# Performance work log

Hardware: AMD Instinct MI355X
Metric: run time of the kernel (lower is better)

Reference implementation:

```python
import jax, jax.numpy as jnp
import numpy as np

CLAMP_MIN = 1e-12
CLAMP_MAX = 1e12


def setup_inputs() -> dict:
    key = jax.random.key(0)
    k1, k2, k3 = jax.random.split(key, 3)
    N, D, C = 16384, 512, 10000
    features = jax.random.normal(k1, (N, D), dtype=jnp.float32)
    labels = jax.random.randint(k2, (N, 2), 0, C, dtype=jnp.int64)
    # torch.rand -> uniform [0,1)
    centers = jax.random.uniform(k3, (C, D), dtype=jnp.float32)
    return {"features": features, "labels": labels, "centers": centers}


def reference(features, labels, centers):
    # labels[:, -1] selects the class id per sample
    cls = labels[:, -1]
    # Original computes full cdist(features, centers)**2 then masks to the
    # label-matched entry per row. Mathematically that is ||f_i - c_{y_i}||^2,
    # so we gather the matching center and reduce directly (O(N*D)).
    c = centers[cls]                      # [N, D] gather
    diff = features - c                   # [N, D]
    d2 = jnp.sum(diff * diff, axis=-1)    # [N] squared L2 distance
    d2 = jnp.clip(d2, CLAMP_MIN, CLAMP_MAX)
    return jnp.mean(d2)
```

## Files before the change

### kernel.cpp

```cpp
#include <hip/hip_runtime.h>

#define N_ROWS 16384
#define DIM 512
#define NBLK 2048
#define NTHR 256
#define WAVES_PER_BLK (NTHR / 64)
#define ROWS_PER_WAVE 2


__global__ __launch_bounds__(NTHR, 8) void centerloss_partial(
    const float* __restrict__ features,
    const int* __restrict__ labels,
    const float* __restrict__ centers,
    float* __restrict__ partials)
{
    const int lane = threadIdx.x & 63;
    const int wid  = threadIdx.x >> 6;
    const int gwave = blockIdx.x * WAVES_PER_BLK + wid;
    const int base  = gwave * ROWS_PER_WAVE;

    int cls0 = labels[(base + 0) * 2 + 1];
    int cls1 = labels[(base + 1) * 2 + 1];

    const float4* __restrict__ f4 =
        reinterpret_cast<const float4*>(features + (size_t)base * DIM);
    float4 fa0 = f4[lane +   0];  float4 fb0 = f4[lane +  64];
    float4 fa1 = f4[lane + 128];  float4 fb1 = f4[lane + 192];

    const float4* __restrict__ c0 =
        reinterpret_cast<const float4*>(centers + (size_t)cls0 * DIM);
    const float4* __restrict__ c1 =
        reinterpret_cast<const float4*>(centers + (size_t)cls1 * DIM);
    float4 ca0 = c0[lane];  float4 cb0 = c0[lane + 64];
    float4 ca1 = c1[lane];  float4 cb1 = c1[lane + 64];

    float lsum = 0.f, dx;
    dx = fa0.x - ca0.x; lsum += dx * dx;
    dx = fa0.y - ca0.y; lsum += dx * dx;
    dx = fa0.z - ca0.z; lsum += dx * dx;
    dx = fa0.w - ca0.w; lsum += dx * dx;
    dx = fb0.x - cb0.x; lsum += dx * dx;
    dx = fb0.y - cb0.y; lsum += dx * dx;
    dx = fb0.z - cb0.z; lsum += dx * dx;
    dx = fb0.w - cb0.w; lsum += dx * dx;

    dx = fa1.x - ca1.x; lsum += dx * dx;
    dx = fa1.y - ca1.y; lsum += dx * dx;
    dx = fa1.z - ca1.z; lsum += dx * dx;
    dx = fa1.w - ca1.w; lsum += dx * dx;
    dx = fb1.x - cb1.x; lsum += dx * dx;
    dx = fb1.y - cb1.y; lsum += dx * dx;
    dx = fb1.z - cb1.z; lsum += dx * dx;
    dx = fb1.w - cb1.w; lsum += dx * dx;

    #pragma unroll
    for (int off = 1; off < 64; off <<= 1)
        lsum += __shfl_xor(lsum, off, 64);

    __shared__ float smem[WAVES_PER_BLK];
    if (lane == 0) smem[wid] = lsum;
    __syncthreads();
    if (threadIdx.x == 0) {
        float b = 0.f;
        #pragma unroll
        for (int w = 0; w < WAVES_PER_BLK; ++w) b += smem[w];
        partials[blockIdx.x] = b;
    }
}

__global__ __launch_bounds__(256) void centerloss_final(
    const float* __restrict__ partials, float* __restrict__ out)
{
    float s = 0.f;
    #pragma unroll
    for (int k = 0; k < NBLK / 256; ++k)
        s += partials[threadIdx.x + k * 256];

    #pragma unroll
    for (int off = 1; off < 64; off <<= 1)
        s += __shfl_xor(s, off, 64);

    __shared__ float smem[4];
    const int lane = threadIdx.x & 63;
    const int wave = threadIdx.x >> 6;
    if (lane == 0) smem[wave] = s;
    __syncthreads();
    if (threadIdx.x == 0) {
        float t = smem[0] + smem[1] + smem[2] + smem[3];
        out[0] = t / (float)N_ROWS;
    }
}

extern "C" void kernel_launch(void* const* d_in, const int* in_sizes, int n_in,
                              void* d_out, int out_size, void* d_ws, size_t ws_size,
                              hipStream_t stream)
{
    const float* features = (const float*)d_in[0];
    const int*   labels   = (const int*)d_in[1];
    const float* centers  = (const float*)d_in[2];
    float* out = (float*)d_out;
    float* partials = (float*)d_ws;

    centerloss_partial<<<NBLK, NTHR, 0, stream>>>(features, labels, centers, partials);
    centerloss_final<<<1, 256, 0, stream>>>(partials, out);
}
```

Baseline: 16.92 us.

## Use single-wave blocks with four rows each and nontemporal feature loads

The partial kernel now runs one 64-thread wave per block and has each wave process four rows instead of two, which removes the LDS reduction and the block barrier. Feature loads use nontemporal hints so the streamed data does not pollute the cache, and the squared differences accumulate in a 4-wide vector before a final horizontal add. The final kernel reads the 4096 partials as float4. In exchange, more loads are in flight per wave but there are fewer waves in total, and single-wave blocks may limit occupancy per CU.

```diff
diff --git a/kernel.cpp b/kernel.cpp
--- a/kernel.cpp
+++ b/kernel.cpp
@@ -2,79 +2,80 @@
 
 #define N_ROWS 16384
 #define DIM 512
-#define NBLK 2048
-#define NTHR 256
-#define WAVES_PER_BLK (NTHR / 64)
-#define ROWS_PER_WAVE 2
+#define NBLK 4096
+#define ROWS_PER_WAVE 4
+
+typedef float f32x4 __attribute__((ext_vector_type(4)));
 
 
-__global__ __launch_bounds__(NTHR, 8) void centerloss_partial(
+__global__ __launch_bounds__(64) void centerloss_partial(
     const float* __restrict__ features,
     const int* __restrict__ labels,
     const float* __restrict__ centers,
     float* __restrict__ partials)
 {
-    const int lane = threadIdx.x & 63;
-    const int wid  = threadIdx.x >> 6;
-    const int gwave = blockIdx.x * WAVES_PER_BLK + wid;
-    const int base  = gwave * ROWS_PER_WAVE;
+    const int lane = threadIdx.x;
+    const int base = blockIdx.x * ROWS_PER_WAVE;
 
     int cls0 = labels[(base + 0) * 2 + 1];
     int cls1 = labels[(base + 1) * 2 + 1];
+    int cls2 = labels[(base + 2) * 2 + 1];
+    int cls3 = labels[(base + 3) * 2 + 1];
 
-    const float4* __restrict__ f4 =
-        reinterpret_cast<const float4*>(features + (size_t)base * DIM);
-    float4 fa0 = f4[lane +   0];  float4 fb0 = f4[lane +  64];
-    float4 fa1 = f4[lane + 128];  float4 fb1 = f4[lane + 192];
+    const f32x4* __restrict__ f4 =
+        reinterpret_cast<const f32x4*>(features + (size_t)base * DIM);
+    f32x4 fa0 = __builtin_nontemporal_load(&f4[lane +   0]);
+    f32x4 fb0 = __builtin_nontemporal_load(&f4[lane +  64]);
+    f32x4 fa1 = __builtin_nontemporal_load(&f4[lane + 128]);
+    f32x4 fb1 = __builtin_nontemporal_load(&f4[lane + 192]);
+    f32x4 fa2 = __builtin_nontemporal_load(&f4[lane + 256]);
+    f32x4 fb2 = __builtin_nontemporal_load(&f4[lane + 320]);
+    f32x4 fa3 = __builtin_nontemporal_load(&f4[lane + 384]);
+    f32x4 fb3 = __builtin_nontemporal_load(&f4[lane + 448]);
 
-    const float4* __restrict__ c0 =
-        reinterpret_cast<const float4*>(centers + (size_t)cls0 * DIM);
-    const float4* __restrict__ c1 =
-        reinterpret_cast<const float4*>(centers + (size_t)cls1 * DIM);
-    float4 ca0 = c0[lane];  float4 cb0 = c0[lane + 64];
-    float4 ca1 = c1[lane];  float4 cb1 = c1[lane + 64];
+    const f32x4* __restrict__ c0 =
+        reinterpret_cast<const f32x4*>(centers + (size_t)cls0 * DIM);
+    const f32x4* __restrict__ c1 =
+        reinterpret_cast<const f32x4*>(centers + (size_t)cls1 * DIM);
+    const f32x4* __restrict__ c2 =
+        reinterpret_cast<const f32x4*>(centers + (size_t)cls2 * DIM);
+    const f32x4* __restrict__ c3 =
+        reinterpret_cast<const f32x4*>(centers + (size_t)cls3 * DIM);
+    f32x4 ca0 = c0[lane];  f32x4 cb0 = c0[lane + 64];
+    f32x4 ca1 = c1[lane];  f32x4 cb1 = c1[lane + 64];
+    f32x4 ca2 = c2[lane];  f32x4 cb2 = c2[lane + 64];
+    f32x4 ca3 = c3[lane];  f32x4 cb3 = c3[lane + 64];
 
-    float lsum = 0.f, dx;
-    dx = fa0.x - ca0.x; lsum += dx * dx;
-    dx = fa0.y - ca0.y; lsum += dx * dx;
-    dx = fa0.z - ca0.z; lsum += dx * dx;
-    dx = fa0.w - ca0.w; lsum += dx * dx;
-    dx = fb0.x - cb0.x; lsum += dx * dx;
-    dx = fb0.y - cb0.y; lsum += dx * dx;
-    dx = fb0.z - cb0.z; lsum += dx * dx;
-    dx = fb0.w - cb0.w; lsum += dx * dx;
+    f32x4 d;
+    f32x4 vsum;
+    d = fa0 - ca0; vsum  = d * d;
+    d = fb0 - cb0; vsum += d * d;
+    d = fa1 - ca1; vsum += d * d;
+    d = fb1 - cb1; vsum += d * d;
+    d = fa2 - ca2; vsum += d * d;
+    d = fb2 - cb2; vsum += d * d;
+    d = fa3 - ca3; vsum += d * d;
+    d = fb3 - cb3; vsum += d * d;
 
-    dx = fa1.x - ca1.x; lsum += dx * dx;
-    dx = fa1.y - ca1.y; lsum += dx * dx;
-    dx = fa1.z - ca1.z; lsum += dx * dx;
-    dx = fa1.w - ca1.w; lsum += dx * dx;
-    dx = fb1.x - cb1.x; lsum += dx * dx;
-    dx = fb1.y - cb1.y; lsum += dx * dx;
-    dx = fb1.z - cb1.z; lsum += dx * dx;
-    dx = fb1.w - cb1.w; lsum += dx * dx;
+    float lsum = vsum.x + vsum.y + vsum.z + vsum.w;
 
     #pragma unroll
     for (int off = 1; off < 64; off <<= 1)
         lsum += __shfl_xor(lsum, off, 64);
 
-    __shared__ float smem[WAVES_PER_BLK];
-    if (lane == 0) smem[wid] = lsum;
-    __syncthreads();
-    if (threadIdx.x == 0) {
-        float b = 0.f;
-        #pragma unroll
-        for (int w = 0; w < WAVES_PER_BLK; ++w) b += smem[w];
-        partials[blockIdx.x] = b;
-    }
+    if (lane == 0) partials[blockIdx.x] = lsum;
 }
 
 __global__ __launch_bounds__(256) void centerloss_final(
     const float* __restrict__ partials, float* __restrict__ out)
 {
+    const float4* __restrict__ p4 = reinterpret_cast<const float4*>(partials);
     float s = 0.f;
     #pragma unroll
-    for (int k = 0; k < NBLK / 256; ++k)
-        s += partials[threadIdx.x + k * 256];
+    for (int k = 0; k < NBLK / 4 / 256; ++k) {
+        float4 v = p4[threadIdx.x + k * 256];
+        s += v.x + v.y + v.z + v.w;
+    }
 
     #pragma unroll
     for (int off = 1; off < 64; off <<= 1)
@@ -101,6 +102,6 @@
     float* out = (float*)d_out;
     float* partials = (float*)d_ws;
 
-    centerloss_partial<<<NBLK, NTHR, 0, stream>>>(features, labels, centers, partials);
+    centerloss_partial<<<NBLK, 64, 0, stream>>>(features, labels, centers, partials);
     centerloss_final<<<1, 256, 0, stream>>>(partials, out);
 }
```

Result: faster. 16.38 us (-3.2%).
